# Kernel tuning notes

Hardware: AMD Instinct MI355X
Metric: run time of the kernel (lower is better)

Reference implementation:

```python
import jax, jax.numpy as jnp
import numpy as np

ST_HIDDEN = 128
ST_HEADS = 4
ST_LAYERS = 3
RES_SCALE = 1.0
DK = ST_HIDDEN // ST_HEADS


def build_3d_adj(spatial_ei, spatial_ea, n_nodes, window):
    # replicate spatial edges per time slice with node offset t*n_nodes
    offs = (jnp.arange(window) * n_nodes)[None, :, None]  # [1,W,1]
    all_sp_idx = (spatial_ei[:, None, :] + offs).reshape(2, -1)  # [2, W*E]
    all_sp_attr = jnp.tile(spatial_ea, (window, 1))  # [W*E, De]
    # temporal edges t -> t+1 for every node
    src = jnp.arange((window - 1) * n_nodes)
    temp_idx = jnp.stack([src, src + n_nodes], axis=0)  # [2, (W-1)*N]
    temp_attr = jnp.broadcast_to(spatial_ea.mean(axis=0, keepdims=True),
                                 (temp_idx.shape[1], spatial_ea.shape[1]))
    ei = jnp.concatenate([all_sp_idx, temp_idx], axis=1)
    ea = jnp.concatenate([all_sp_attr, temp_attr], axis=0)
    return ei, ea


def seg_softmax(logits, dst, num_nodes):
    # logits [E,H], segment softmax over dst (pyg_softmax)
    m = jax.ops.segment_max(logits, dst, num_segments=num_nodes)  # [N,H]
    ex = jnp.exp(logits - m[dst])
    s = jax.ops.segment_sum(ex, dst, num_segments=num_nodes)
    return ex / (s[dst] + 1e-16)


def layernorm(x, g, b, eps=1e-5):
    mu = x.mean(-1, keepdims=True)
    var = ((x - mu) ** 2).mean(-1, keepdims=True)
    return (x - mu) * jax.lax.rsqrt(var + eps) * g + b


def block(x, ei, ea, qw, qb, kw, kb, vw, vb, fw, fb, ow, ob, ln_g, ln_b):
    B, Nt, _ = x.shape
    H, dk = ST_HEADS, DK
    Q = (x @ qw + qb).reshape(B, Nt, H, dk)
    K = (x @ kw + kb).reshape(B, Nt, H, dk)
    V = (x @ vw + vb).reshape(B, Nt, H, dk)
    src, dst = ei[0], ei[1]
    q_e = Q[:, dst]  # [B,E,H,dk]
    k_e = K[:, src]
    v_e = V[:, src]
    film = ea @ fw + fb  # [E, 2*hidden]
    gamma, beta = jnp.split(film, 2, axis=-1)
    gamma = gamma.reshape(1, -1, H, dk)
    beta = beta.reshape(1, -1, H, dk)
    k_e = k_e * (1.0 + gamma) + beta
    logits = (q_e * k_e).sum(-1) / np.sqrt(dk).astype(np.float32)  # [B,E,H]
    att = jax.vmap(lambda l: seg_softmax(l, dst, Nt))(logits)
    msg = att[..., None] * v_e  # [B,E,H,dk]
    out = jnp.zeros((B, Nt, H, dk), x.dtype).at[:, dst].add(msg)
    y = out.reshape(B, Nt, H * dk) @ ow + ob
    return layernorm(x + y, ln_g, ln_b)


def setup_inputs() -> dict:
    key = jax.random.key(0)
    ks = jax.random.split(key, 12)
    B, W, N, Fin, E, De = 2, 16, 1000, 16, 16000, 8
    H, L = ST_HIDDEN, ST_LAYERS
    g = lambda k, s: jax.random.normal(k, s, jnp.float32) * 0.05
    return {
        "xw": jax.random.normal(ks[0], (B, W, N, Fin), jnp.float32),
        "spatial_ei": jax.random.randint(ks[1], (2, E), 0, N),
        "spatial_ea": jax.random.normal(ks[2], (E, De), jnp.float32),
        "in_w": g(ks[3], (Fin, H)), "in_b": jnp.zeros((H,), jnp.float32),
        "qw": g(ks[4], (L, H, H)), "qb": jnp.zeros((L, H), jnp.float32),
        "kw": g(ks[5], (L, H, H)), "kb": jnp.zeros((L, H), jnp.float32),
        "vw": g(ks[6], (L, H, H)), "vb": jnp.zeros((L, H), jnp.float32),
        "fw": g(ks[7], (L, De, 2 * H)), "fb": jnp.zeros((L, 2 * H), jnp.float32),
        "ow": g(ks[8], (L, H, H)), "ob": jnp.zeros((L, H), jnp.float32),
        "ln_g": jnp.ones((L, H), jnp.float32), "ln_b": jnp.zeros((L, H), jnp.float32),
        "head_w": g(ks[9], (H, 1)), "head_b": jnp.zeros((1,), jnp.float32),
    }


def reference(xw, spatial_ei, spatial_ea, in_w, in_b, qw, qb, kw, kb, vw, vb,
              fw, fb, ow, ob, ln_g, ln_b, head_w, head_b):
    B, W, N, Fin = xw.shape
    ei, ea = build_3d_adj(spatial_ei, spatial_ea, N, W)
    x = xw.reshape(B, W * N, Fin) @ in_w + in_b
    for l in range(ST_LAYERS):
        bx = block(x, ei, ea, qw[l], qb[l], kw[l], kb[l], vw[l], vb[l],
                   fw[l], fb[l], ow[l], ob[l], ln_g[l], ln_b[l])
        x = x + RES_SCALE * (bx - x)
    last = x.reshape(B, W, N, -1)[:, -1]  # [B,N,H]
    return jax.nn.softplus(last @ head_w + head_b).squeeze(-1)  # [B,N]
```

## Files before the change

kernel.cpp:

```cpp
#include <hip/hip_runtime.h>
#include <math.h>

constexpr int B    = 2;
constexpr int W    = 16;
constexpr int N    = 1000;
constexpr int FIN  = 16;
constexpr int E    = 16000;
constexpr int DE   = 8;
constexpr int H    = 128;
constexpr int L    = 3;
constexpr int WL   = 4;
constexpr int W0G  = 12;
constexpr int RPB  = WL * N;
constexpr int ROWS = B * RPB;
constexpr int NMAT = 12;
constexpr int NFILM = (E + 1 + 7) / 8;

__device__ __forceinline__ float dot4(float4 a, float4 b) {
  return a.x * b.x + a.y * b.y + a.z * b.z + a.w * b.w;
}
__device__ __forceinline__ float dpp_add_xor1(float x) {
  int y = __builtin_amdgcn_update_dpp(0, __float_as_int(x), 0xB1, 0xF, 0xF, true);
  return x + __int_as_float(y);
}
__device__ __forceinline__ float dpp_add_xor2(float x) {
  int y = __builtin_amdgcn_update_dpp(0, __float_as_int(x), 0x4E, 0xF, 0xF, true);
  return x + __int_as_float(y);
}
__device__ __forceinline__ float headSum32(float p) {
  p = dpp_add_xor1(p);
  p = dpp_add_xor2(p);
  p += __shfl_xor(p, 4);
  p += __shfl_xor(p, 8);
  p += __shfl_xor(p, 16);
  return p;
}

__global__ void k_prep(const int* __restrict__ ei, const float* __restrict__ ea,
                       const float* __restrict__ qw, const float* __restrict__ kw,
                       const float* __restrict__ vw, const float* __restrict__ ow,
                       float4* __restrict__ wTp4,
                       const float* __restrict__ xw, const float* __restrict__ in_w,
                       const float* __restrict__ in_b, float* __restrict__ x,
                       float* __restrict__ meanea, int* __restrict__ offs,
                       int* __restrict__ cursor) {
  __shared__ union {
    struct { int cnt[1024]; int sT[256]; } sc;
    struct { float xwS[64][FIN]; float inS[FIN][H]; } ip;
    float sbuf[256];
  } sm;
  int bid = blockIdx.x;
  int t = threadIdx.x;
  if (bid == 0) {
    int* cnt = sm.sc.cnt;
    for (int i = t; i < 1024; i += 256) cnt[i] = 0;
    __syncthreads();
    for (int e0 = t; e0 < E; e0 += 1024) {
      int v[4];
      #pragma unroll
      for (int j = 0; j < 4; j++) {
        int e = e0 + j * 256;
        v[j] = (e < E) ? ei[E + e] : -1;
      }
      #pragma unroll
      for (int j = 0; j < 4; j++) if (v[j] >= 0) atomicAdd(&cnt[v[j]], 1);
    }
    __syncthreads();
    int idx0 = t * 4;
    int c0 = cnt[idx0], c1 = cnt[idx0 + 1], c2 = cnt[idx0 + 2], c3 = cnt[idx0 + 3];
    int run = c0 + c1 + c2 + c3;
    int* sT = sm.sc.sT;
    sT[t] = run;
    __syncthreads();
    for (int st = 1; st < 256; st <<= 1) {
      int add = (t >= st) ? sT[t - st] : 0;
      __syncthreads();
      sT[t] += add;
      __syncthreads();
    }
    int pos = sT[t] - run;
    int cs[4] = {c0, c1, c2, c3};
    #pragma unroll
    for (int j = 0; j < 4; j++) {
      int i = idx0 + j;
      if (i < N) { offs[i + 1] = pos + cs[j]; cursor[i] = pos; }
      pos += cs[j];
    }
    if (t == 0) offs[0] = 0;
  } else if (bid < 49) {
    int u0 = (bid - 1) * 1024;
    #pragma unroll
    for (int q = 0; q < 4; q++) {
      int o = u0 + q * 256 + t;
      int mat = o >> 12, rem = o & 4095;
      int kk4 = rem >> 7, c = rem & 127;
      int l = mat >> 2, mm = mat & 3;
      const float* src = ((mm == 0) ? qw : (mm == 1) ? kw : (mm == 2) ? vw : ow)
                         + (long)l * H * H;
      int k0 = kk4 * 4;
      float4 v4 = make_float4(src[(k0 + 0) * H + c], src[(k0 + 1) * H + c],
                              src[(k0 + 2) * H + c], src[(k0 + 3) * H + c]);
      wTp4[o] = v4;
    }
  } else if (bid < 81) {
    int eb = bid - 49;
    int d = t & 7, g = t >> 3;
    float s = 0.f;
    for (int e = eb * 32 + g; e < E; e += 32 * 32) s += ea[e * DE + d];
    sm.sbuf[t] = s;
    __syncthreads();
    for (int st = 16; st >= 1; st >>= 1) {
      if (g < st) sm.sbuf[g * 8 + d] += sm.sbuf[(g + st) * 8 + d];
      __syncthreads();
    }
    if (g == 0) atomicAdd(&meanea[d], sm.sbuf[d]);
  } else {
    int bi = bid - 81;
    int b = bi / 63, tt = bi % 63;
    int lr0 = tt * 64;
    for (int i = t; i < 64 * FIN; i += 256) {
      int r = i >> 4, k = i & 15;
      int lr = lr0 + r;
      float val = 0.f;
      if (lr < RPB) {
        int wl = lr / N, n = lr % N;
        val = xw[(((long)b * W + (W0G + wl)) * N + n) * FIN + k];
      }
      sm.ip.xwS[r][k] = val;
    }
    for (int i = t; i < FIN * H; i += 256) sm.ip.inS[i >> 7][i & 127] = in_w[i];
    __syncthreads();
    #pragma unroll
    for (int qi = 0; qi < 8; qi++) {
      int idx = t + qi * 256;
      int r = idx >> 5, cq = idx & 31;
      int lr = lr0 + r;
      if (lr < RPB) {
        float4 acc = *(const float4*)(in_b + cq * 4);
        #pragma unroll
        for (int k = 0; k < FIN; k++) {
          float xv = sm.ip.xwS[r][k];
          float4 w4 = *(const float4*)(&sm.ip.inS[k][cq * 4]);
          acc.x += xv * w4.x; acc.y += xv * w4.y; acc.z += xv * w4.z; acc.w += xv * w4.w;
        }
        *(float4*)(x + ((long)b * RPB + lr) * H + cq * 4) = acc;
      }
    }
  }
}

__global__ void k_mid(const float* __restrict__ X, const float4* __restrict__ wTp4,
                      int matBase,
                      const float* __restrict__ bq, const float* __restrict__ bk,
                      const float* __restrict__ bv,
                      float* __restrict__ Cq, float* __restrict__ Ck, float* __restrict__ Cv,
                      int base, int rows_pb, int tiles, int nG,
                      const float* __restrict__ ea, const float* __restrict__ fwl,
                      const float* __restrict__ fbl, const float* __restrict__ meanea,
                      unsigned int* __restrict__ filmh,
                      const int* __restrict__ ei, int* __restrict__ cursor,
                      int2* __restrict__ csr) {
  __shared__ float xs[32][H];
  int u = blockIdx.x;
  int t = threadIdx.x;
  if (u < nG) {
    int m = u / (B * tiles);
    int r2 = u % (B * tiles);
    int bb = r2 / tiles, tt = r2 % tiles;
    const float* bm = (m == 0) ? bq : (m == 1) ? bk : bv;
    float* Cm       = (m == 0) ? Cq : (m == 1) ? Ck : Cv;
    const float4* wp = wTp4 + (long)(matBase + m) * 32 * H;
    int lr0 = tt * 32;
    long grow0 = (long)bb * RPB + base + lr0;
    #pragma unroll
    for (int qi = 0; qi < 4; qi++) {
      int idx = t + qi * 256;
      int r = idx >> 5, c4 = idx & 31;
      float4 v4 = make_float4(0.f, 0.f, 0.f, 0.f);
      if (lr0 + r < rows_pb) v4 = *(const float4*)(X + (grow0 + r) * H + c4 * 4);
      *(float4*)&xs[r][c4 * 4] = v4;
    }
    __syncthreads();
    int cg = t & 31, rg = t >> 5;
    float4 bias4 = *(const float4*)(bm + cg * 4);
    float4 acc0 = bias4, acc1 = bias4, acc2 = bias4, acc3 = bias4;
    #pragma unroll 4
    for (int kk4 = 0; kk4 < 32; kk4++) {
      const float4* wr = wp + kk4 * H + cg * 4;
      float4 w0 = wr[0], w1 = wr[1], w2 = wr[2], w3 = wr[3];
      float4 x0 = *(const float4*)&xs[rg * 4 + 0][kk4 * 4];
      float4 x1 = *(const float4*)&xs[rg * 4 + 1][kk4 * 4];
      float4 x2 = *(const float4*)&xs[rg * 4 + 2][kk4 * 4];
      float4 x3 = *(const float4*)&xs[rg * 4 + 3][kk4 * 4];
      acc0.x += dot4(x0, w0); acc0.y += dot4(x0, w1); acc0.z += dot4(x0, w2); acc0.w += dot4(x0, w3);
      acc1.x += dot4(x1, w0); acc1.y += dot4(x1, w1); acc1.z += dot4(x1, w2); acc1.w += dot4(x1, w3);
      acc2.x += dot4(x2, w0); acc2.y += dot4(x2, w1); acc2.z += dot4(x2, w2); acc2.w += dot4(x2, w3);
      acc3.x += dot4(x3, w0); acc3.y += dot4(x3, w1); acc3.z += dot4(x3, w2); acc3.w += dot4(x3, w3);
    }
    int lrr = lr0 + rg * 4;
    if (lrr + 0 < rows_pb) *(float4*)(Cm + (grow0 + rg * 4 + 0) * H + cg * 4) = acc0;
    if (lrr + 1 < rows_pb) *(float4*)(Cm + (grow0 + rg * 4 + 1) * H + cg * 4) = acc1;
    if (lrr + 2 < rows_pb) *(float4*)(Cm + (grow0 + rg * 4 + 2) * H + cg * 4) = acc2;
    if (lrr + 3 < rows_pb) *(float4*)(Cm + (grow0 + rg * 4 + 3) * H + cg * 4) = acc3;
  } else if (u < nG + NFILM) {
    int ru = u - nG;
    int c = t & 127, g2 = t >> 7;
    float rgw[DE], rbw[DE];
    #pragma unroll
    for (int d = 0; d < DE; d++) {
      rgw[d] = fwl[d * 2 * H + c];
      rbw[d] = fwl[d * 2 * H + H + c];
    }
    float fbg = fbl[c], fbb = fbl[H + c];
    int e0 = ru * 8 + g2 * 4;
    for (int e = e0; e < e0 + 4; e++) {
      if (e > E) break;
      float a[DE];
      if (e < E) {
        float4 a0 = *(const float4*)(ea + (long)e * DE);
        float4 a1 = *(const float4*)(ea + (long)e * DE + 4);
        a[0] = a0.x; a[1] = a0.y; a[2] = a0.z; a[3] = a0.w;
        a[4] = a1.x; a[5] = a1.y; a[6] = a1.z; a[7] = a1.w;
      } else {
        #pragma unroll
        for (int d = 0; d < DE; d++) a[d] = meanea[d] * (1.0f / E);
      }
      float g = fbg, be = fbb;
      #pragma unroll
      for (int d = 0; d < DE; d++) {
        g  += a[d] * rgw[d];
        be += a[d] * rbw[d];
      }
      unsigned int gb = __float_as_uint(g);
      gb = (gb + 0x7fffu + ((gb >> 16) & 1u)) >> 16;
      unsigned int bb_ = __float_as_uint(be);
      bb_ = (bb_ + 0x7fffu + ((bb_ >> 16) & 1u)) & 0xffff0000u;
      filmh[(long)e * H + c] = gb | bb_;
    }
  } else {
    int f = u - nG - NFILM;
    int e = f * 256 + t;
    if (e < E) {
      int src = ei[e];
      int dst = ei[E + e];
      int pos = atomicAdd(&cursor[dst], 1);
      csr[pos] = make_int2(src, e);
    }
  }
}

__global__ void k_attn_oln(const float* __restrict__ Qb, const float* __restrict__ Kb,
                           const float* __restrict__ Vb,
                           const unsigned int* __restrict__ filmh,
                           const int* __restrict__ offs, const int2* __restrict__ csr,
                           const float* __restrict__ x, const float4* __restrict__ owp,
                           const float* __restrict__ ob, const float* __restrict__ lng,
                           const float* __restrict__ lnb, float* __restrict__ xo,
                           int out_lo,
                           const float* __restrict__ hw, const float* __restrict__ hb,
                           float* __restrict__ out, int do_head) {
  __shared__ float sab[2][H];
  __shared__ float red[2][2];
  int t = threadIdx.x;
  int half = t >> 7, tid = t & 127;
  int idx = blockIdx.x * 2 + half;
  int nwin = WL - out_lo;
  int b = idx / (nwin * N);
  int rem = idx % (nwin * N);
  int wl = out_lo + rem / N;
  int n = rem % N;
  long drow = ((long)b * WL + wl) * N + n;
  float q = Qb[drow * H + tid];
  long sbase = ((long)b * WL + wl) * N;
  long trow  = ((long)b * WL + wl - 1) * N + n;
  const float scale = 0.17677669529663687f;
  int i0 = offs[n], i1 = offs[n + 1];

  unsigned int fh = filmh[(long)E * H + tid];
  float g  = __uint_as_float(fh << 16);
  float be = __uint_as_float(fh & 0xffff0000u);
  float kv = Kb[trow * H + tid];
  float vv = Vb[trow * H + tid];
  float pp = q * (kv * (1.f + g) + be);
  float pe = __expf(headSum32(pp) * scale);
  float ssum = pe, acc = pe * vv;

  for (int i4 = i0; i4 < i1; i4 += 4) {
    #pragma unroll
    for (int j = 0; j < 4; j++) {
      int i = i4 + j;
      int ic = (i < i1) ? i : (i1 - 1);
      int2 se = csr[ic];
      long srow = sbase + se.x;
      unsigned int f2 = filmh[(long)se.y * H + tid];
      float g2 = __uint_as_float(f2 << 16);
      float b2 = __uint_as_float(f2 & 0xffff0000u);
      float kv2 = Kb[srow * H + tid];
      float vv2 = Vb[srow * H + tid];
      float p2  = q * (kv2 * (1.f + g2) + b2);
      float pe2 = __expf(headSum32(p2) * scale);
      pe2 = (i < i1) ? pe2 : 0.f;
      ssum += pe2;
      acc  += pe2 * vv2;
    }
  }
  float ab = acc / (ssum + 1e-16f);

  sab[half][tid] = ab;
  __syncthreads();
  float y = ob[tid];
  #pragma unroll 8
  for (int kk4 = 0; kk4 < 32; kk4++) {
    float4 w4 = owp[kk4 * H + tid];
    float4 a4 = *(const float4*)&sab[half][kk4 * 4];
    y += dot4(a4, w4);
  }

  float v = x[drow * H + tid] + y;
  #pragma unroll
  for (int off = 32; off >= 1; off >>= 1) v += 0.f;
  float s = x[drow * H + tid] + y;
  float r1 = s;
  #pragma unroll
  for (int off = 32; off >= 1; off >>= 1) r1 += __shfl_xor(r1, off);
  {
    int w = (t >> 6) & 1;
    __syncthreads();
    if ((t & 63) == 0) red[half][w] = r1;
    __syncthreads();
  }
  float mu = (red[half][0] + red[half][1]) * (1.f / H);
  float dv = s - mu;
  float r2v = dv * dv;
  #pragma unroll
  for (int off = 32; off >= 1; off >>= 1) r2v += __shfl_xor(r2v, off);
  {
    int w = (t >> 6) & 1;
    __syncthreads();
    if ((t & 63) == 0) red[half][w] = r2v;
    __syncthreads();
  }
  float var = (red[half][0] + red[half][1]) * (1.f / H);
  float o = dv * rsqrtf(var + 1e-5f) * lng[tid] + lnb[tid];

  if (!do_head) {
    xo[drow * H + tid] = o;
  } else {
    float hv = o * hw[tid];
    float r3 = hv;
    #pragma unroll
    for (int off = 32; off >= 1; off >>= 1) r3 += __shfl_xor(r3, off);
    int w = (t >> 6) & 1;
    __syncthreads();
    if ((t & 63) == 0) red[half][w] = r3;
    __syncthreads();
    if (tid == 0) {
      float z = red[half][0] + red[half][1] + hb[0];
      out[b * N + n] = fmaxf(z, 0.f) + log1pf(expf(-fabsf(z)));
    }
  }
}

extern "C" void kernel_launch(void* const* d_in, const int* in_sizes, int n_in,
                              void* d_out, int out_size, void* d_ws, size_t ws_size,
                              hipStream_t stream) {
  const float* xw   = (const float*)d_in[0];
  const int*   ei   = (const int*)d_in[1];
  const float* ea   = (const float*)d_in[2];
  const float* in_w = (const float*)d_in[3];
  const float* in_b = (const float*)d_in[4];
  const float* qw   = (const float*)d_in[5];
  const float* qb   = (const float*)d_in[6];
  const float* kw   = (const float*)d_in[7];
  const float* kb   = (const float*)d_in[8];
  const float* vw   = (const float*)d_in[9];
  const float* vb   = (const float*)d_in[10];
  const float* fw   = (const float*)d_in[11];
  const float* fb   = (const float*)d_in[12];
  const float* ow   = (const float*)d_in[13];
  const float* ob   = (const float*)d_in[14];
  const float* ln_g = (const float*)d_in[15];
  const float* ln_b = (const float*)d_in[16];
  const float* hw   = (const float*)d_in[17];
  const float* hb   = (const float*)d_in[18];
  float* out = (float*)d_out;

  float* ws   = (float*)d_ws;
  float* x    = ws;
  float* x2   = x  + (long)ROWS * H;
  float* Qb   = x2 + (long)ROWS * H;
  float* Kb   = Qb + (long)ROWS * H;
  float* Vb   = Kb + (long)ROWS * H;
  float* wTp  = Vb + (long)ROWS * H;
  unsigned int* filmh = (unsigned int*)(wTp + (long)NMAT * H * H);
  float* meanea = (float*)(filmh + (long)(E + 1) * H);
  int* offs    = (int*)(meanea + 8);
  int* cursor  = offs + N + 1;
  int2* csr    = (int2*)(cursor + N);
  float4* wTp4 = (float4*)wTp;

  hipMemsetAsync(meanea, 0, 8 * sizeof(float), stream);
  k_prep<<<207, 256, 0, stream>>>(ei, ea, qw, kw, vw, ow, wTp4,
                                  xw, in_w, in_b, x, meanea, offs, cursor);

  float* xa = x;
  float* xb = x2;
  for (int l = 0; l < L; l++) {
    int out_lo = l + 1;
    int rows_pb = (WL - l) * N;
    int tiles = (rows_pb + 31) / 32;
    int nG = 3 * B * tiles;
    int nFill = (l == 0) ? (E + 255) / 256 : 0;
    int nMid = nG + NFILM + nFill;
    k_mid<<<nMid, 256, 0, stream>>>(
        xa, wTp4, l * 4, qb + (long)l * H, kb + (long)l * H, vb + (long)l * H,
        Qb, Kb, Vb, l * N, rows_pb, tiles, nG,
        ea, fw + (long)l * DE * 2 * H, fb + (long)l * 2 * H, meanea, filmh,
        ei, cursor, csr);
    int nout = B * (WL - out_lo) * N;
    int last = (l == L - 1) ? 1 : 0;
    k_attn_oln<<<nout / 2, 256, 0, stream>>>(
        Qb, Kb, Vb, filmh, offs, csr,
        xa, wTp4 + ((long)l * 4 + 3) * 32 * H, ob + (long)l * H,
        ln_g + (long)l * H, ln_b + (long)l * H, xb, out_lo,
        hw, hb, out, last);
    float* tmp = xa; xa = xb; xb = tmp;
  }
}
```

Baseline: 269.1 us.

## Interleave K and V into one buffer and fuse K/V projection blocks

K and V projections are now computed by the same block, which stages the x tile once and writes K and V interleaved per channel into a single KV buffer. The attention kernel then gathers one float2 per edge instead of two separate scalar loads from different rows, and its edge loop is unrolled by 8 instead of 4. This cuts the number of projection blocks and redundant x staging, and halves the number of gather transactions per neighbour. The fused K/V block keeps twice as many accumulators in registers, which may lower occupancy, and the dead no-op reduction loop is removed.

```diff
diff --git a/kernel.cpp b/kernel.cpp
--- a/kernel.cpp
+++ b/kernel.cpp
@@ -153,8 +153,8 @@
                       int matBase,
                       const float* __restrict__ bq, const float* __restrict__ bk,
                       const float* __restrict__ bv,
-                      float* __restrict__ Cq, float* __restrict__ Ck, float* __restrict__ Cv,
-                      int base, int rows_pb, int tiles, int nG,
+                      float* __restrict__ Cq, float* __restrict__ KV,
+                      int base, int rows_pb, int tiles, int nT,
                       const float* __restrict__ ea, const float* __restrict__ fwl,
                       const float* __restrict__ fbl, const float* __restrict__ meanea,
                       unsigned int* __restrict__ filmh,
@@ -163,13 +163,10 @@
   __shared__ float xs[32][H];
   int u = blockIdx.x;
   int t = threadIdx.x;
-  if (u < nG) {
-    int m = u / (B * tiles);
-    int r2 = u % (B * tiles);
+  if (u < 2 * nT) {
+    int role = u / nT;
+    int r2 = u % nT;
     int bb = r2 / tiles, tt = r2 % tiles;
-    const float* bm = (m == 0) ? bq : (m == 1) ? bk : bv;
-    float* Cm       = (m == 0) ? Cq : (m == 1) ? Ck : Cv;
-    const float4* wp = wTp4 + (long)(matBase + m) * 32 * H;
     int lr0 = tt * 32;
     long grow0 = (long)bb * RPB + base + lr0;
     #pragma unroll
@@ -182,28 +179,68 @@
     }
     __syncthreads();
     int cg = t & 31, rg = t >> 5;
-    float4 bias4 = *(const float4*)(bm + cg * 4);
-    float4 acc0 = bias4, acc1 = bias4, acc2 = bias4, acc3 = bias4;
-    #pragma unroll 4
-    for (int kk4 = 0; kk4 < 32; kk4++) {
-      const float4* wr = wp + kk4 * H + cg * 4;
-      float4 w0 = wr[0], w1 = wr[1], w2 = wr[2], w3 = wr[3];
-      float4 x0 = *(const float4*)&xs[rg * 4 + 0][kk4 * 4];
-      float4 x1 = *(const float4*)&xs[rg * 4 + 1][kk4 * 4];
-      float4 x2 = *(const float4*)&xs[rg * 4 + 2][kk4 * 4];
-      float4 x3 = *(const float4*)&xs[rg * 4 + 3][kk4 * 4];
-      acc0.x += dot4(x0, w0); acc0.y += dot4(x0, w1); acc0.z += dot4(x0, w2); acc0.w += dot4(x0, w3);
-      acc1.x += dot4(x1, w0); acc1.y += dot4(x1, w1); acc1.z += dot4(x1, w2); acc1.w += dot4(x1, w3);
-      acc2.x += dot4(x2, w0); acc2.y += dot4(x2, w1); acc2.z += dot4(x2, w2); acc2.w += dot4(x2, w3);
-      acc3.x += dot4(x3, w0); acc3.y += dot4(x3, w1); acc3.z += dot4(x3, w2); acc3.w += dot4(x3, w3);
-    }
-    int lrr = lr0 + rg * 4;
-    if (lrr + 0 < rows_pb) *(float4*)(Cm + (grow0 + rg * 4 + 0) * H + cg * 4) = acc0;
-    if (lrr + 1 < rows_pb) *(float4*)(Cm + (grow0 + rg * 4 + 1) * H + cg * 4) = acc1;
-    if (lrr + 2 < rows_pb) *(float4*)(Cm + (grow0 + rg * 4 + 2) * H + cg * 4) = acc2;
-    if (lrr + 3 < rows_pb) *(float4*)(Cm + (grow0 + rg * 4 + 3) * H + cg * 4) = acc3;
-  } else if (u < nG + NFILM) {
-    int ru = u - nG;
+    if (role == 0) {
+      const float4* wp = wTp4 + (long)(matBase + 0) * 32 * H;
+      float4 bias4 = *(const float4*)(bq + cg * 4);
+      float4 a0 = bias4, a1 = bias4, a2 = bias4, a3 = bias4;
+      #pragma unroll 4
+      for (int kk4 = 0; kk4 < 32; kk4++) {
+        const float4* wr = wp + kk4 * H + cg * 4;
+        float4 w0 = wr[0], w1 = wr[1], w2 = wr[2], w3 = wr[3];
+        float4 x0 = *(const float4*)&xs[rg * 4 + 0][kk4 * 4];
+        float4 x1 = *(const float4*)&xs[rg * 4 + 1][kk4 * 4];
+        float4 x2 = *(const float4*)&xs[rg * 4 + 2][kk4 * 4];
+        float4 x3 = *(const float4*)&xs[rg * 4 + 3][kk4 * 4];
+        a0.x += dot4(x0, w0); a0.y += dot4(x0, w1); a0.z += dot4(x0, w2); a0.w += dot4(x0, w3);
+        a1.x += dot4(x1, w0); a1.y += dot4(x1, w1); a1.z += dot4(x1, w2); a1.w += dot4(x1, w3);
+        a2.x += dot4(x2, w0); a2.y += dot4(x2, w1); a2.z += dot4(x2, w2); a2.w += dot4(x2, w3);
+        a3.x += dot4(x3, w0); a3.y += dot4(x3, w1); a3.z += dot4(x3, w2); a3.w += dot4(x3, w3);
+      }
+      int lrr = lr0 + rg * 4;
+      if (lrr + 0 < rows_pb) *(float4*)(Cq + (grow0 + rg * 4 + 0) * H + cg * 4) = a0;
+      if (lrr + 1 < rows_pb) *(float4*)(Cq + (grow0 + rg * 4 + 1) * H + cg * 4) = a1;
+      if (lrr + 2 < rows_pb) *(float4*)(Cq + (grow0 + rg * 4 + 2) * H + cg * 4) = a2;
+      if (lrr + 3 < rows_pb) *(float4*)(Cq + (grow0 + rg * 4 + 3) * H + cg * 4) = a3;
+    } else {
+      const float4* wpk = wTp4 + (long)(matBase + 1) * 32 * H;
+      const float4* wpv = wTp4 + (long)(matBase + 2) * 32 * H;
+      float4 bk4 = *(const float4*)(bk + cg * 4);
+      float4 bv4 = *(const float4*)(bv + cg * 4);
+      float4 k0 = bk4, k1 = bk4, k2 = bk4, k3 = bk4;
+      float4 v0 = bv4, v1 = bv4, v2 = bv4, v3 = bv4;
+      #pragma unroll 2
+      for (int kk4 = 0; kk4 < 32; kk4++) {
+        const float4* wrk = wpk + kk4 * H + cg * 4;
+        const float4* wrv = wpv + kk4 * H + cg * 4;
+        float4 wk0 = wrk[0], wk1 = wrk[1], wk2 = wrk[2], wk3 = wrk[3];
+        float4 wv0 = wrv[0], wv1 = wrv[1], wv2 = wrv[2], wv3 = wrv[3];
+        float4 x0 = *(const float4*)&xs[rg * 4 + 0][kk4 * 4];
+        float4 x1 = *(const float4*)&xs[rg * 4 + 1][kk4 * 4];
+        float4 x2 = *(const float4*)&xs[rg * 4 + 2][kk4 * 4];
+        float4 x3 = *(const float4*)&xs[rg * 4 + 3][kk4 * 4];
+        k0.x += dot4(x0, wk0); k0.y += dot4(x0, wk1); k0.z += dot4(x0, wk2); k0.w += dot4(x0, wk3);
+        k1.x += dot4(x1, wk0); k1.y += dot4(x1, wk1); k1.z += dot4(x1, wk2); k1.w += dot4(x1, wk3);
+        k2.x += dot4(x2, wk0); k2.y += dot4(x2, wk1); k2.z += dot4(x2, wk2); k2.w += dot4(x2, wk3);
+        k3.x += dot4(x3, wk0); k3.y += dot4(x3, wk1); k3.z += dot4(x3, wk2); k3.w += dot4(x3, wk3);
+        v0.x += dot4(x0, wv0); v0.y += dot4(x0, wv1); v0.z += dot4(x0, wv2); v0.w += dot4(x0, wv3);
+        v1.x += dot4(x1, wv0); v1.y += dot4(x1, wv1); v1.z += dot4(x1, wv2); v1.w += dot4(x1, wv3);
+        v2.x += dot4(x2, wv0); v2.y += dot4(x2, wv1); v2.z += dot4(x2, wv2); v2.w += dot4(x2, wv3);
+        v3.x += dot4(x3, wv0); v3.y += dot4(x3, wv1); v3.z += dot4(x3, wv2); v3.w += dot4(x3, wv3);
+      }
+      int lrr = lr0 + rg * 4;
+      float4 ks[4] = {k0, k1, k2, k3};
+      float4 vs[4] = {v0, v1, v2, v3};
+      #pragma unroll
+      for (int i = 0; i < 4; i++) {
+        if (lrr + i < rows_pb) {
+          float* bp = KV + (grow0 + rg * 4 + i) * (2 * H) + cg * 8;
+          *(float4*)bp       = make_float4(ks[i].x, vs[i].x, ks[i].y, vs[i].y);
+          *(float4*)(bp + 4) = make_float4(ks[i].z, vs[i].z, ks[i].w, vs[i].w);
+        }
+      }
+    }
+  } else if (u < 2 * nT + NFILM) {
+    int ru = u - 2 * nT;
     int c = t & 127, g2 = t >> 7;
     float rgw[DE], rbw[DE];
     #pragma unroll
@@ -238,7 +275,7 @@
       filmh[(long)e * H + c] = gb | bb_;
     }
   } else {
-    int f = u - nG - NFILM;
+    int f = u - 2 * nT - NFILM;
     int e = f * 256 + t;
     if (e < E) {
       int src = ei[e];
@@ -249,8 +286,7 @@
   }
 }
 
-__global__ void k_attn_oln(const float* __restrict__ Qb, const float* __restrict__ Kb,
-                           const float* __restrict__ Vb,
+__global__ void k_attn_oln(const float* __restrict__ Qb, const float* __restrict__ KV,
                            const unsigned int* __restrict__ filmh,
                            const int* __restrict__ offs, const int2* __restrict__ csr,
                            const float* __restrict__ x, const float4* __restrict__ owp,
@@ -279,29 +315,27 @@
   unsigned int fh = filmh[(long)E * H + tid];
   float g  = __uint_as_float(fh << 16);
   float be = __uint_as_float(fh & 0xffff0000u);
-  float kv = Kb[trow * H + tid];
-  float vv = Vb[trow * H + tid];
-  float pp = q * (kv * (1.f + g) + be);
+  float2 kvt = *(const float2*)(KV + trow * (2 * H) + tid * 2);
+  float pp = q * (kvt.x * (1.f + g) + be);
   float pe = __expf(headSum32(pp) * scale);
-  float ssum = pe, acc = pe * vv;
-
-  for (int i4 = i0; i4 < i1; i4 += 4) {
-    #pragma unroll
-    for (int j = 0; j < 4; j++) {
-      int i = i4 + j;
+  float ssum = pe, acc = pe * kvt.y;
+
+  for (int i8 = i0; i8 < i1; i8 += 8) {
+    #pragma unroll
+    for (int j = 0; j < 8; j++) {
+      int i = i8 + j;
       int ic = (i < i1) ? i : (i1 - 1);
       int2 se = csr[ic];
       long srow = sbase + se.x;
       unsigned int f2 = filmh[(long)se.y * H + tid];
       float g2 = __uint_as_float(f2 << 16);
       float b2 = __uint_as_float(f2 & 0xffff0000u);
-      float kv2 = Kb[srow * H + tid];
-      float vv2 = Vb[srow * H + tid];
-      float p2  = q * (kv2 * (1.f + g2) + b2);
+      float2 kv2 = *(const float2*)(KV + srow * (2 * H) + tid * 2);
+      float p2  = q * (kv2.x * (1.f + g2) + b2);
       float pe2 = __expf(headSum32(p2) * scale);
       pe2 = (i < i1) ? pe2 : 0.f;
       ssum += pe2;
-      acc  += pe2 * vv2;
+      acc  += pe2 * kv2.y;
     }
   }
   float ab = acc / (ssum + 1e-16f);
@@ -316,9 +350,6 @@
     y += dot4(a4, w4);
   }
 
-  float v = x[drow * H + tid] + y;
-  #pragma unroll
-  for (int off = 32; off >= 1; off >>= 1) v += 0.f;
   float s = x[drow * H + tid] + y;
   float r1 = s;
   #pragma unroll
@@ -389,9 +420,8 @@
   float* x    = ws;
   float* x2   = x  + (long)ROWS * H;
   float* Qb   = x2 + (long)ROWS * H;
-  float* Kb   = Qb + (long)ROWS * H;
-  float* Vb   = Kb + (long)ROWS * H;
-  float* wTp  = Vb + (long)ROWS * H;
+  float* KVb  = Qb + (long)ROWS * H;
+  float* wTp  = KVb + (long)ROWS * 2 * H;
   unsigned int* filmh = (unsigned int*)(wTp + (long)NMAT * H * H);
   float* meanea = (float*)(filmh + (long)(E + 1) * H);
   int* offs    = (int*)(meanea + 8);
@@ -409,18 +439,18 @@
     int out_lo = l + 1;
     int rows_pb = (WL - l) * N;
     int tiles = (rows_pb + 31) / 32;
-    int nG = 3 * B * tiles;
+    int nT = B * tiles;
     int nFill = (l == 0) ? (E + 255) / 256 : 0;
-    int nMid = nG + NFILM + nFill;
+    int nMid = 2 * nT + NFILM + nFill;
     k_mid<<<nMid, 256, 0, stream>>>(
         xa, wTp4, l * 4, qb + (long)l * H, kb + (long)l * H, vb + (long)l * H,
-        Qb, Kb, Vb, l * N, rows_pb, tiles, nG,
+        Qb, KVb, l * N, rows_pb, tiles, nT,
         ea, fw + (long)l * DE * 2 * H, fb + (long)l * 2 * H, meanea, filmh,
         ei, cursor, csr);
     int nout = B * (WL - out_lo) * N;
     int last = (l == L - 1) ? 1 : 0;
     k_attn_oln<<<nout / 2, 256, 0, stream>>>(
-        Qb, Kb, Vb, filmh, offs, csr,
+        Qb, KVb, filmh, offs, csr,
         xa, wTp4 + ((long)l * 4 + 3) * 32 * H, ob + (long)l * H,
         ln_g + (long)l * H, ln_b + (long)l * H, xb, out_lo,
         hw, hb, out, last);
```

Result: no change. 273.7 us (+1.7%).
